# Kernel tuning notes

Hardware: AMD Instinct MI355X
Metric: run time of the kernel (lower is better)

Reference implementation:

```python
import jax, jax.numpy as jnp
import numpy as np
from jax import lax

SEQ_LEN = 4096
INPUT_SIZE = 1024
HIDDEN = 1024
NUM_CLASSES = 3


def setup_inputs() -> dict:
    key = jax.random.key(0)
    ks = jax.random.split(key, 12)
    s = 1.0 / np.sqrt(HIDDEN)  # torch LSTM/Linear uniform init scale
    def u(k, shape):
        return jax.random.uniform(k, shape, jnp.float32, -s, s)
    inp = jax.random.normal(ks[0], (SEQ_LEN, 1, INPUT_SIZE), jnp.float32)
    return {
        "inp": inp,
        # forward-direction LSTM params (gate order i,f,g,o as in torch)
        "Wih_f": u(ks[1], (4 * HIDDEN, INPUT_SIZE)),
        "Whh_f": u(ks[2], (4 * HIDDEN, HIDDEN)),
        "bih_f": u(ks[3], (4 * HIDDEN,)),
        "bhh_f": u(ks[4], (4 * HIDDEN,)),
        # backward-direction LSTM params
        "Wih_b": u(ks[5], (4 * HIDDEN, INPUT_SIZE)),
        "Whh_b": u(ks[6], (4 * HIDDEN, HIDDEN)),
        "bih_b": u(ks[7], (4 * HIDDEN,)),
        "bhh_b": u(ks[8], (4 * HIDDEN,)),
        # output head: Linear(2*HIDDEN, 3)
        "W_ho": u(ks[9], (NUM_CLASSES, 2 * HIDDEN)),
        "b_ho": u(ks[10], (NUM_CLASSES,)),
    }


def _lstm_last_h(x, Wih, Whh, bih, bhh):
    # x: (T, B, I) -> final hidden state (B, H)
    H = Whh.shape[1]
    B = x.shape[1]
    bias = bih + bhh
    # precompute input projections for all timesteps: (T, B, 4H)
    xg = jnp.einsum('tbi,gi->tbg', x, Wih) + bias

    def step(carry, xt):
        h, c = carry
        gates = xt + h @ Whh.T  # (B, 4H)
        i, f, g, o = jnp.split(gates, 4, axis=-1)
        c = jax.nn.sigmoid(f) * c + jax.nn.sigmoid(i) * jnp.tanh(g)
        h = jax.nn.sigmoid(o) * jnp.tanh(c)
        return (h, c), None

    init = (jnp.zeros((B, H), x.dtype), jnp.zeros((B, H), x.dtype))
    (hT, _), _ = lax.scan(step, init, xg)
    return hT


def reference(inp, Wih_f, Whh_f, bih_f, bhh_f, Wih_b, Whh_b, bih_b, bhh_b, W_ho, b_ho):
    h_fwd = _lstm_last_h(inp, Wih_f, Whh_f, bih_f, bhh_f)          # (1, H)
    h_bwd = _lstm_last_h(inp[::-1], Wih_b, Whh_b, bih_b, bhh_b)    # (1, H)
    hidden = jnp.concatenate([h_fwd, h_bwd], axis=-1)              # (1, 2H)
    # Dropout(p=0.35) is identity in eval mode.
    return hidden @ W_ho.T + b_ho                                  # (1, 3)
```

## Files before the change

kernel.cpp:

```cpp
#include <hip/hip_runtime.h>
#include <stdint.h>


#define T_SEQ 4096
#define ISZ   1024
#define HID   1024
#define NB_TOT 256
#define NTHR  512
#define PAD   68

typedef unsigned long long u64;
typedef unsigned int u32;

__device__ __forceinline__ float fast_sigmoid(float x) {
    return 1.0f / (1.0f + __expf(-x));
}
__device__ __forceinline__ float fast_tanh(float x) {
    return 1.0f - 2.0f / (__expf(2.0f * x) + 1.0f);
}
__device__ __forceinline__ float h16f(unsigned short u) {
    _Float16 h; __builtin_memcpy(&h, &u, 2); return (float)h;
}
__device__ __forceinline__ unsigned short fh16(float f) {
    _Float16 h = (_Float16)f; unsigned short u; __builtin_memcpy(&u, &h, 2); return u;
}

#define PIN4(v) asm volatile("" : "+v"(v.x), "+v"(v.y), "+v"(v.z), "+v"(v.w))
#define DOT4(a, b) ((a).x*(b).x + (a).y*(b).y + (a).z*(b).z + (a).w*(b).w)

#define GM 64
#define GN 64
#define GK 32

__global__ __launch_bounds__(256)
void xproj_gemm(const float* __restrict__ x,
                const float* __restrict__ Wih_f, const float* __restrict__ bih_f,
                const float* __restrict__ bhh_f,
                const float* __restrict__ Wih_b, const float* __restrict__ bih_b,
                const float* __restrict__ bhh_b,
                float* __restrict__ xg)
{
    const int dir = blockIdx.z;
    const float* Wih = dir ? Wih_b : Wih_f;
    const float* bih = dir ? bih_b : bih_f;
    const float* bhh = dir ? bhh_b : bhh_f;
    const int m0 = blockIdx.y * GM;
    const int n0 = blockIdx.x * GN;
    const int tid = threadIdx.x;
    const int ms = tid >> 2;
    const int kq = tid & 3;
    const int tm = tid >> 4;
    const int tn = tid & 15;

    __shared__ float As[GK][GM + 4];
    __shared__ float Bs[GK][GN + 4];

    float acc[4][4] = {};

    const int mrow = m0 + ms;
    const int xrow = dir ? (T_SEQ - 1 - mrow) : mrow;
    const float* ap = x + (size_t)xrow * ISZ + kq * 8;
    const float* bp = Wih + (size_t)(n0 + ms) * ISZ + kq * 8;

    for (int k0 = 0; k0 < ISZ; k0 += GK) {
        float4 a0 = *(const float4*)(ap + k0);
        float4 a1 = *(const float4*)(ap + k0 + 4);
        float4 b0 = *(const float4*)(bp + k0);
        float4 b1 = *(const float4*)(bp + k0 + 4);
        __syncthreads();
        const int kb = kq * 8;
        As[kb+0][ms]=a0.x; As[kb+1][ms]=a0.y; As[kb+2][ms]=a0.z; As[kb+3][ms]=a0.w;
        As[kb+4][ms]=a1.x; As[kb+5][ms]=a1.y; As[kb+6][ms]=a1.z; As[kb+7][ms]=a1.w;
        Bs[kb+0][ms]=b0.x; Bs[kb+1][ms]=b0.y; Bs[kb+2][ms]=b0.z; Bs[kb+3][ms]=b0.w;
        Bs[kb+4][ms]=b1.x; Bs[kb+5][ms]=b1.y; Bs[kb+6][ms]=b1.z; Bs[kb+7][ms]=b1.w;
        __syncthreads();
        #pragma unroll
        for (int k = 0; k < GK; ++k) {
            float4 av = *(const float4*)&As[k][tm * 4];
            float4 bv = *(const float4*)&Bs[k][tn * 4];
            acc[0][0] += av.x*bv.x; acc[0][1] += av.x*bv.y; acc[0][2] += av.x*bv.z; acc[0][3] += av.x*bv.w;
            acc[1][0] += av.y*bv.x; acc[1][1] += av.y*bv.y; acc[1][2] += av.y*bv.z; acc[1][3] += av.y*bv.w;
            acc[2][0] += av.z*bv.x; acc[2][1] += av.z*bv.y; acc[2][2] += av.z*bv.z; acc[2][3] += av.z*bv.w;
            acc[3][0] += av.w*bv.x; acc[3][1] += av.w*bv.y; acc[3][2] += av.w*bv.z; acc[3][3] += av.w*bv.w;
        }
    }

    const int gc = n0 + tn * 4;
    float4 bb1 = *(const float4*)(bih + gc);
    float4 bb2 = *(const float4*)(bhh + gc);
    float bx = bb1.x + bb2.x, by = bb1.y + bb2.y, bz = bb1.z + bb2.z, bw = bb1.w + bb2.w;
    float* op = xg + ((size_t)dir << 24) + (size_t)(m0 + tm * 4) * 4096 + gc;
    #pragma unroll
    for (int i = 0; i < 4; ++i) {
        float4 v;
        v.x = acc[i][0] + bx; v.y = acc[i][1] + by;
        v.z = acc[i][2] + bz; v.w = acc[i][3] + bw;
        *(float4*)(op + (size_t)i * 4096) = v;
    }
}

__global__ __attribute__((amdgpu_flat_work_group_size(NTHR, NTHR)))
           __attribute__((amdgpu_waves_per_eu(2, 2)))
void bilstm_rec(const float* __restrict__ xg,
                const float* __restrict__ Whh_f, const float* __restrict__ Whh_b,
                u32* hpack)
{
    const int tid = threadIdx.x;
    const int blk = blockIdx.x;
    const int dir = blk >> 7;
    const int lb  = blk & 127;
    const int u0  = lb * 8;
    const int w   = tid >> 6;
    const int l   = tid & 63;
    const int q   = l >> 4;
    const int kc  = l & 15;
    const int unit = u0 + w;
    const int grow = q * HID + unit;

    const float* Whh = dir ? Whh_b : Whh_f;
    const float* xgd = xg + ((size_t)dir << 24);
    u32* hp = hpack + (size_t)dir * 2 * HID;

    __shared__ __align__(16) float lds_h[2][16 * PAD];

    const float* wp = Whh + (size_t)grow * HID + kc * 64;
    float4 w0 = *(const float4*)(wp + 0),  w1 = *(const float4*)(wp + 4);
    float4 w2 = *(const float4*)(wp + 8),  w3 = *(const float4*)(wp + 12);
    float4 w4 = *(const float4*)(wp + 16), w5 = *(const float4*)(wp + 20);
    float4 w6 = *(const float4*)(wp + 24), w7 = *(const float4*)(wp + 28);
    float4 w8 = *(const float4*)(wp + 32), w9 = *(const float4*)(wp + 36);
    float4 wa = *(const float4*)(wp + 40), wb = *(const float4*)(wp + 44);
    float4 wc = *(const float4*)(wp + 48), wd = *(const float4*)(wp + 52);
    float4 we = *(const float4*)(wp + 56), wf = *(const float4*)(wp + 60);
    PIN4(w0); PIN4(w1); PIN4(w2); PIN4(w3);
    PIN4(w4); PIN4(w5); PIN4(w6); PIN4(w7);
    PIN4(w8); PIN4(w9); PIN4(wa); PIN4(wb);
    PIN4(wc); PIN4(wd); PIN4(we); PIN4(wf);

    const float a_scl = (q == 2) ? 2.0f : 1.0f;
    const float a_mul = (q == 2) ? 2.0f : 1.0f;
    const float a_add = (q == 2) ? -1.0f : 0.0f;

    float c_state = 0.0f;
    float xgv = 0.0f;
    if (kc == 0) xgv = xgd[grow];
    asm volatile("" : "+v"(xgv));

    bool dead = false;

    for (int t = 0; t < T_SEQ; ++t) {
        float s = 0.0f;

        if (t > 0) {
            const int b = (t - 1) & 1;
            const u64* src = (const u64*)(hp + (size_t)b * HID) + tid;
            const unsigned tg = (unsigned)t & 0xFFFFu;
            u64 e = 0;
            if (!dead) {
                int sp = 0;
                for (;;) {
                    e = __hip_atomic_load(src, __ATOMIC_RELAXED,
                                          __HIP_MEMORY_SCOPE_AGENT);
                    if ((((unsigned)(e >> 16) & 0xFFFFu) == tg) &
                        ((unsigned)(e >> 48) == tg)) break;
                    if (++sp > (1 << 21)) { dead = true; break; }
                    __builtin_amdgcn_s_sleep(1);
                }
            }
            const int k0 = tid * 2;
            float2 hv;
            hv.x = h16f((unsigned short)(e & 0xFFFFu));
            hv.y = h16f((unsigned short)((e >> 32) & 0xFFFFu));
            *(float2*)&lds_h[b][(k0 >> 6) * PAD + (k0 & 63)] = hv;
            __syncthreads();

            const float* lh = &lds_h[b][kc * PAD];
            float4 h0 = *(const float4*)(lh + 0),  h1 = *(const float4*)(lh + 4);
            float4 h2 = *(const float4*)(lh + 8),  h3 = *(const float4*)(lh + 12);
            float4 h4 = *(const float4*)(lh + 16), h5 = *(const float4*)(lh + 20);
            float4 h6 = *(const float4*)(lh + 24), h7 = *(const float4*)(lh + 28);
            s  = DOT4(w0,h0) + DOT4(w1,h1) + DOT4(w2,h2) + DOT4(w3,h3);
            s += DOT4(w4,h4) + DOT4(w5,h5) + DOT4(w6,h6) + DOT4(w7,h7);
            float4 h8 = *(const float4*)(lh + 32), h9 = *(const float4*)(lh + 36);
            float4 ha = *(const float4*)(lh + 40), hb = *(const float4*)(lh + 44);
            float4 hc = *(const float4*)(lh + 48), hd = *(const float4*)(lh + 52);
            float4 he = *(const float4*)(lh + 56), hf = *(const float4*)(lh + 60);
            s += DOT4(w8,h8) + DOT4(w9,h9) + DOT4(wa,ha) + DOT4(wb,hb);
            s += DOT4(wc,hc) + DOT4(wd,hd) + DOT4(we,he) + DOT4(wf,hf);
        }

        s += __shfl_xor(s, 1);
        s += __shfl_xor(s, 2);
        s += __shfl_xor(s, 4);
        s += __shfl_xor(s, 8);

        float pg = s + xgv;
        float act = a_mul * fast_sigmoid(a_scl * pg) + a_add;

        float sf = __shfl(act, 16);
        float tg2 = __shfl(act, 32);
        float so = __shfl(act, 48);

        if (l == 0) {
            float si = act;
            c_state = sf * c_state + si * tg2;
            float hval = so * fast_tanh(c_state);
            u32 pk = (((u32)(t + 1) & 0xFFFFu) << 16) | (u32)fh16(hval);
            __hip_atomic_store(hp + (size_t)(t & 1) * HID + unit, pk,
                               __ATOMIC_RELAXED, __HIP_MEMORY_SCOPE_AGENT);
        }
        asm volatile("s_waitcnt vmcnt(0)" ::: "memory");

        if (t + 1 < T_SEQ && kc == 0) {
            xgv = xgd[(size_t)(t + 1) * 4096 + grow];
            asm volatile("" : "+v"(xgv));
        }
    }
}

__global__ void head_kernel(const float* __restrict__ W_ho,
                            const float* __restrict__ b_ho,
                            const u32* __restrict__ hpack,
                            float* __restrict__ out)
{
    const u32* hf  = hpack + 1 * HID;
    const u32* hbk = hpack + 3 * HID;
    __shared__ float r0[4], r1[4], r2[4];
    int tid = threadIdx.x;
    float p0 = 0.f, p1 = 0.f, p2 = 0.f;
    for (int i = tid; i < 2 * HID; i += 256) {
        u32 e = (i < HID) ? hf[i] : hbk[i - HID];
        _Float16 hh; unsigned short us = (unsigned short)(e & 0xFFFFu);
        __builtin_memcpy(&hh, &us, 2);
        float hv = (float)hh;
        p0 += W_ho[0 * 2 * HID + i] * hv;
        p1 += W_ho[1 * 2 * HID + i] * hv;
        p2 += W_ho[2 * 2 * HID + i] * hv;
    }
    #pragma unroll
    for (int m = 1; m < 64; m <<= 1) {
        p0 += __shfl_xor(p0, m);
        p1 += __shfl_xor(p1, m);
        p2 += __shfl_xor(p2, m);
    }
    int w = tid >> 6;
    if ((tid & 63) == 0) { r0[w] = p0; r1[w] = p1; r2[w] = p2; }
    __syncthreads();
    if (tid == 0) {
        out[0] = b_ho[0] + r0[0] + r0[1] + r0[2] + r0[3];
        out[1] = b_ho[1] + r1[0] + r1[1] + r1[2] + r1[3];
        out[2] = b_ho[2] + r2[0] + r2[1] + r2[2] + r2[3];
    }
}

extern "C" void kernel_launch(void* const* d_in, const int* in_sizes, int n_in,
                              void* d_out, int out_size, void* d_ws, size_t ws_size,
                              hipStream_t stream) {
    const float* x     = (const float*)d_in[0];
    const float* Wih_f = (const float*)d_in[1];
    const float* Whh_f = (const float*)d_in[2];
    const float* bih_f = (const float*)d_in[3];
    const float* bhh_f = (const float*)d_in[4];
    const float* Wih_b = (const float*)d_in[5];
    const float* Whh_b = (const float*)d_in[6];
    const float* bih_b = (const float*)d_in[7];
    const float* bhh_b = (const float*)d_in[8];
    const float* W_ho  = (const float*)d_in[9];
    const float* b_ho  = (const float*)d_in[10];

    u32* hpack = (u32*)d_ws;
    float* xg = (float*)((char*)d_ws + 32768);

    hipMemsetAsync(d_ws, 0, 2 * 2 * HID * sizeof(u32), stream);

    dim3 gg(4096 / GN, T_SEQ / GM, 2);
    xproj_gemm<<<gg, 256, 0, stream>>>(x, Wih_f, bih_f, bhh_f,
                                       Wih_b, bih_b, bhh_b, xg);
    bilstm_rec<<<NB_TOT, NTHR, 0, stream>>>(xg, Whh_f, Whh_b, hpack);
    head_kernel<<<1, 256, 0, stream>>>(W_ho, b_ho, hpack, (float*)d_out);
}
```

Baseline: 7.998 ms.

## Compute input projection with fp16 MFMA GEMM after converting operands to half

Adds kernels that convert the input sequence and both input-weight matrices to fp16 in workspace, then computes the all-timestep input projections with a 64x64-tile GEMM using 16x16x32 f16 MFMA instructions, accumulating in fp32. This replaces the fp32 scalar GEMM when the workspace is large enough, and the old path is kept as a fallback. The goal is to cut the cost of the large projection GEMM. In exchange it adds conversion passes and extra workspace traffic, and fp16 rounding of inputs and weights may affect accuracy. The recurrent kernel, which likely dominates total time, is unchanged.

```diff
diff --git a/kernel.cpp b/kernel.cpp
--- a/kernel.cpp
+++ b/kernel.cpp
@@ -11,6 +11,8 @@
 
 typedef unsigned long long u64;
 typedef unsigned int u32;
+typedef _Float16 half8 __attribute__((ext_vector_type(8)));
+typedef float f32x4 __attribute__((ext_vector_type(4)));
 
 __device__ __forceinline__ float fast_sigmoid(float x) {
     return 1.0f / (1.0f + __expf(-x));
@@ -27,6 +29,90 @@
 
 #define PIN4(v) asm volatile("" : "+v"(v.x), "+v"(v.y), "+v"(v.z), "+v"(v.w))
 #define DOT4(a, b) ((a).x*(b).x + (a).y*(b).y + (a).z*(b).z + (a).w*(b).w)
+
+__global__ __launch_bounds__(256)
+void f32_to_f16(const float* __restrict__ src, _Float16* __restrict__ dst, int n)
+{
+    int i = (blockIdx.x * 256 + threadIdx.x) * 8;
+    if (i < n) {
+        float4 v0 = *(const float4*)(src + i);
+        float4 v1 = *(const float4*)(src + i + 4);
+        half8 h;
+        h[0] = (_Float16)v0.x; h[1] = (_Float16)v0.y;
+        h[2] = (_Float16)v0.z; h[3] = (_Float16)v0.w;
+        h[4] = (_Float16)v1.x; h[5] = (_Float16)v1.y;
+        h[6] = (_Float16)v1.z; h[7] = (_Float16)v1.w;
+        *(half8*)(dst + i) = h;
+    }
+}
+
+__global__ __launch_bounds__(256)
+void xproj_mfma(const _Float16* __restrict__ x16,
+                const _Float16* __restrict__ w16f, const _Float16* __restrict__ w16b,
+                const float* __restrict__ bih_f, const float* __restrict__ bhh_f,
+                const float* __restrict__ bih_b, const float* __restrict__ bhh_b,
+                float* __restrict__ xg)
+{
+    const int dir = blockIdx.z;
+    const _Float16* W = dir ? w16b : w16f;
+    const float* bih = dir ? bih_b : bih_f;
+    const float* bhh = dir ? bhh_b : bhh_f;
+    const int m0 = blockIdx.y * 64;
+    const int n0 = blockIdx.x * 64;
+    const int tid = threadIdx.x;
+    const int wid = tid >> 6;
+    const int l   = tid & 63;
+    const int wm = (wid >> 1) * 32, wn = (wid & 1) * 32;
+
+    __shared__ _Float16 As[64][40];
+    __shared__ _Float16 Bs[64][40];
+
+    f32x4 acc00 = {}, acc01 = {}, acc10 = {}, acc11 = {};
+
+    const int arow = tid >> 2;
+    const int aseg = (tid & 3) * 8;
+    const int xrow = dir ? (T_SEQ - 1 - (m0 + arow)) : (m0 + arow);
+    const _Float16* ap = x16 + (size_t)xrow * ISZ + aseg;
+    const _Float16* bp = W + (size_t)(n0 + arow) * ISZ + aseg;
+
+    const int fr = l & 15, ko = (l >> 4) * 8;
+
+    for (int k0 = 0; k0 < ISZ; k0 += 32) {
+        half8 av = *(const half8*)(ap + k0);
+        half8 bv = *(const half8*)(bp + k0);
+        __syncthreads();
+        *(half8*)&As[arow][aseg] = av;
+        *(half8*)&Bs[arow][aseg] = bv;
+        __syncthreads();
+        half8 a0 = *(const half8*)&As[wm + fr][ko];
+        half8 a1 = *(const half8*)&As[wm + 16 + fr][ko];
+        half8 b0 = *(const half8*)&Bs[wn + fr][ko];
+        half8 b1 = *(const half8*)&Bs[wn + 16 + fr][ko];
+        acc00 = __builtin_amdgcn_mfma_f32_16x16x32_f16(a0, b0, acc00, 0, 0, 0);
+        acc01 = __builtin_amdgcn_mfma_f32_16x16x32_f16(a0, b1, acc01, 0, 0, 0);
+        acc10 = __builtin_amdgcn_mfma_f32_16x16x32_f16(a1, b0, acc10, 0, 0, 0);
+        acc11 = __builtin_amdgcn_mfma_f32_16x16x32_f16(a1, b1, acc11, 0, 0, 0);
+    }
+
+    const int cc = l & 15, cr = (l >> 4) * 4;
+    float* xgd = xg + ((size_t)dir << 24);
+    #pragma unroll
+    for (int i = 0; i < 2; ++i) {
+        #pragma unroll
+        for (int j = 0; j < 2; ++j) {
+            f32x4 a = (i == 0) ? (j == 0 ? acc00 : acc01)
+                               : (j == 0 ? acc10 : acc11);
+            int gm = m0 + wm + i * 16 + cr;
+            int gn = n0 + wn + j * 16 + cc;
+            float bias = bih[gn] + bhh[gn];
+            float* op = xgd + (size_t)gm * 4096 + gn;
+            op[0]                 = a[0] + bias;
+            op[(size_t)1 * 4096]  = a[1] + bias;
+            op[(size_t)2 * 4096]  = a[2] + bias;
+            op[(size_t)3 * 4096]  = a[3] + bias;
+        }
+    }
+}
 
 #define GM 64
 #define GN 64
@@ -270,12 +356,28 @@
 
     u32* hpack = (u32*)d_ws;
     float* xg = (float*)((char*)d_ws + 32768);
+    const size_t xg_bytes = (size_t)2 * 4096 * 4096 * sizeof(float);
+    char* f16base = (char*)d_ws + 32768 + xg_bytes;
+    _Float16* x16  = (_Float16*)f16base;
+    _Float16* w16f = (_Float16*)(f16base + (size_t)8 * 1024 * 1024);
+    _Float16* w16b = (_Float16*)(f16base + (size_t)16 * 1024 * 1024);
+    const size_t need_mfma = 32768 + xg_bytes + (size_t)24 * 1024 * 1024;
 
     hipMemsetAsync(d_ws, 0, 2 * 2 * HID * sizeof(u32), stream);
 
-    dim3 gg(4096 / GN, T_SEQ / GM, 2);
-    xproj_gemm<<<gg, 256, 0, stream>>>(x, Wih_f, bih_f, bhh_f,
-                                       Wih_b, bih_b, bhh_b, xg);
+    const int NCONV = T_SEQ * ISZ;
+    if (ws_size >= need_mfma) {
+        f32_to_f16<<<NCONV / 8 / 256, 256, 0, stream>>>(x, x16, NCONV);
+        f32_to_f16<<<NCONV / 8 / 256, 256, 0, stream>>>(Wih_f, w16f, NCONV);
+        f32_to_f16<<<NCONV / 8 / 256, 256, 0, stream>>>(Wih_b, w16b, NCONV);
+        dim3 gg(4096 / 64, 4096 / 64, 2);
+        xproj_mfma<<<gg, 256, 0, stream>>>(x16, w16f, w16b,
+                                           bih_f, bhh_f, bih_b, bhh_b, xg);
+    } else {
+        dim3 gg(4096 / GN, T_SEQ / GM, 2);
+        xproj_gemm<<<gg, 256, 0, stream>>>(x, Wih_f, bih_f, bhh_f,
+                                           Wih_b, bih_b, bhh_b, xg);
+    }
     bilstm_rec<<<NB_TOT, NTHR, 0, stream>>>(xg, Whh_f, Whh_b, hpack);
     head_kernel<<<1, 256, 0, stream>>>(W_ho, b_ho, hpack, (float*)d_out);
 }
```

Measured after the change: 7.403 ms, median of 2. 1.08x faster.
